# Kernel optimization log

Measured on AMD Instinct MI355X. Metric: run time of the kernel, lower is better.

The kernel has to match this reference:

```python
import jax, jax.numpy as jnp
import numpy as np


def setup_inputs() -> dict:
    key = jax.random.key(0)
    k1, k2, k3, k4, k5 = jax.random.split(key, 5)
    B, S, DK, D = 64, 2048, 1024, 1024
    hidden_state = jax.random.normal(k1, (B, D), dtype=jnp.float32)
    encoder_outputs = jax.random.normal(k2, (B, S, DK), dtype=jnp.float32)
    # linear1: in = dim_key + dim*num_layers = 2048, out = dim = 1024
    W1 = jax.random.normal(k3, (D, DK + D), dtype=jnp.float32) * (1.0 / np.sqrt(DK + D))
    b1 = jax.random.normal(k4, (D,), dtype=jnp.float32) * 0.01
    W2 = jax.random.normal(k5, (1, D), dtype=jnp.float32) * (1.0 / np.sqrt(D))
    return {"hidden_state": hidden_state, "encoder_outputs": encoder_outputs,
            "W1": W1, "b1": b1, "W2": W2}


def reference(hidden_state, encoder_outputs, W1, b1, W2):
    # torch: cat([enc, h], -1) @ W1.T  ==  enc @ W1e.T + h @ W1h.T
    # (split avoids materializing the [B,S,DK+D] concat; same math)
    DK = encoder_outputs.shape[-1]
    W1e, W1h = W1[:, :DK], W1[:, DK:]
    # pre: [B, S, D]
    pre = (jnp.einsum('bsk,dk->bsd', encoder_outputs, W1e)
           + jnp.einsum('bm,dm->bd', hidden_state, W1h)[:, None, :]
           + b1)
    e = jnp.einsum('bsd,d->bs', jnp.tanh(pre), W2[0])  # scores [B, S]
    alpha = jax.nn.softmax(e, axis=1)
    context = jnp.einsum('bs,bsk->bk', alpha, encoder_outputs)  # [B, DK]
    return context
```

## Files before the change

### kernel.cpp

```cpp
#include <hip/hip_runtime.h>

typedef __attribute__((ext_vector_type(8))) short short8;
typedef __attribute__((ext_vector_type(4))) float floatx4;

#define M_TOT 131072
#define SEQ   2048
#define NB    8

__device__ __forceinline__ unsigned bf16rne(float x) {
  unsigned u = __float_as_uint(x);
  return (u + 0x7FFFu + ((u >> 16) & 1u)) >> 16;
}

#define GLOAD_LDS16(g, l) __builtin_amdgcn_global_load_lds( \
    (const __attribute__((address_space(1))) unsigned int*)(g), \
    (__attribute__((address_space(3))) unsigned int*)(l), 16, 0, 0)

__global__ __launch_bounds__(256) void convert_enc_kernel(
    const float* __restrict__ in, unsigned int* __restrict__ out)
{
  size_t i = ((size_t)blockIdx.x * 256 + threadIdx.x) * 8;
  float4 a = *(const float4*)(in + i);
  float4 b = *(const float4*)(in + i + 4);
  uint4 o;
  o.x = bf16rne(a.x) | (bf16rne(a.y) << 16);
  o.y = bf16rne(a.z) | (bf16rne(a.w) << 16);
  o.z = bf16rne(b.x) | (bf16rne(b.y) << 16);
  o.w = bf16rne(b.z) | (bf16rne(b.w) << 16);
  *(uint4*)(out + i / 2) = o;
}

__global__ __launch_bounds__(128) void convert_w1e_kernel(
    const float* __restrict__ W1, unsigned int* __restrict__ out)
{
  int d = blockIdx.x;
  int k = threadIdx.x * 8;
  const float* p = W1 + (size_t)d * 2048 + k;
  float4 a = *(const float4*)p;
  float4 b = *(const float4*)(p + 4);
  uint4 o;
  o.x = bf16rne(a.x) | (bf16rne(a.y) << 16);
  o.y = bf16rne(a.z) | (bf16rne(a.w) << 16);
  o.z = bf16rne(b.x) | (bf16rne(b.y) << 16);
  o.w = bf16rne(b.z) | (bf16rne(b.w) << 16);
  *(uint4*)(out + ((size_t)d * 1024 + k) / 2) = o;
}

__global__ __launch_bounds__(256) void hvec_kernel(
    const float* __restrict__ hid, const float* __restrict__ W1,
    const float* __restrict__ b1, float* __restrict__ hvec)
{
  int b = blockIdx.x, g = blockIdx.y;
  int w = threadIdx.x >> 6, lane = threadIdx.x & 63;
  const float* hrow = hid + b * 1024;
  for (int i = 0; i < 16; ++i) {
    int d = g * 64 + w * 16 + i;
    const float* wrow = W1 + (size_t)d * 2048 + 1024;
    float sum = 0.f;
#pragma unroll
    for (int c = 0; c < 4; ++c) {
      int m = c * 256 + lane * 4;
      float4 wv = *(const float4*)(wrow + m);
      float4 hv = *(const float4*)(hrow + m);
      sum += wv.x * hv.x + wv.y * hv.y + wv.z * hv.z + wv.w * hv.w;
    }
#pragma unroll
    for (int msk = 1; msk < 64; msk <<= 1) sum += __shfl_xor(sum, msk);
    if (lane == 0) hvec[b * 1024 + d] = sum + b1[d];
  }
}

__global__ __launch_bounds__(512, 2) void gemm256_kernel(
    const unsigned short* __restrict__ A, const unsigned short* __restrict__ B,
    const float* __restrict__ W2, const float* __restrict__ hvec,
    float* __restrict__ epart)
{
  __shared__ __align__(16) unsigned short lds[4][2][8192];

  const int tid = threadIdx.x;
  const int lid = blockIdx.x;
  const int xcd = lid & 7, q = lid >> 3;
  const int mb = xcd * 64 + (q >> 2);
  const int nb = q & 3;
  const int r0 = mb * 256, n0 = nb * 256;
  const int bidx = r0 >> 11;
  const int wid = tid >> 6, lane = tid & 63;
  const int wm = wid >> 2, wn = wid & 3;
  const int lrow = lane & 15, kq = lane >> 4;

  int offA[2], offB[2], dst[2];
#pragma unroll
  for (int j = 0; j < 2; ++j) {
    int c = tid + j * 512;
    int r = c >> 2, s = c & 3;
    offA[j] = (r0 + r) * 1024 + s * 8;
    offB[j] = (n0 + r) * 1024 + s * 8;
    dst[j] = (wid * 64 + j * 512) * 8;
  }

  floatx4 acc[8][4];
#pragma unroll
  for (int i = 0; i < 8; ++i)
#pragma unroll
    for (int j = 0; j < 4; ++j)
      acc[i][j] = (floatx4){0.f, 0.f, 0.f, 0.f};

#define STAGE_J(T, J) do { \
    GLOAD_LDS16(A + (size_t)offA[J] + (T) * 32, &lds[(T) & 3][0][dst[J]]); \
    GLOAD_LDS16(B + (size_t)offB[J] + (T) * 32, &lds[(T) & 3][1][dst[J]]); \
  } while (0)

  STAGE_J(0, 0); STAGE_J(0, 1);
  STAGE_J(1, 0); STAGE_J(1, 1);

  const int aB = wm * 4096 + lrow * 32 + kq * 8;
  const int bB = wn * 2048 + lrow * 32 + kq * 8;

  for (int tt = 0; tt < 8; ++tt) {
#pragma unroll
    for (int u = 0; u < 4; ++u) {
      const int t = tt * 4 + u;
      const unsigned short* Ah = lds[u][0];
      const unsigned short* Bh = lds[u][1];

      if (t >= 30) { asm volatile("s_waitcnt vmcnt(0)" ::: "memory"); }
      else         { asm volatile("s_waitcnt vmcnt(4)" ::: "memory"); }
      __builtin_amdgcn_s_barrier();

      short8 af[8];
#pragma unroll
      for (int mt = 0; mt < 8; ++mt) af[mt] = *(const short8*)&Ah[aB + mt * 512];
      short8 bf0 = *(const short8*)&Bh[bB];
      short8 bf1 = *(const short8*)&Bh[bB + 512];
      if (t < 30) STAGE_J(t + 2, 0);
      __builtin_amdgcn_s_setprio(1);
#pragma unroll
      for (int mt = 0; mt < 8; ++mt) {
        acc[mt][0] = __builtin_amdgcn_mfma_f32_16x16x32_bf16(af[mt], bf0, acc[mt][0], 0, 0, 0);
        acc[mt][1] = __builtin_amdgcn_mfma_f32_16x16x32_bf16(af[mt], bf1, acc[mt][1], 0, 0, 0);
      }
      __builtin_amdgcn_s_setprio(0);
      short8 bf2 = *(const short8*)&Bh[bB + 1024];
      short8 bf3 = *(const short8*)&Bh[bB + 1536];
      if (t < 30) STAGE_J(t + 2, 1);
      __builtin_amdgcn_s_setprio(1);
#pragma unroll
      for (int mt = 0; mt < 8; ++mt) {
        acc[mt][2] = __builtin_amdgcn_mfma_f32_16x16x32_bf16(af[mt], bf2, acc[mt][2], 0, 0, 0);
        acc[mt][3] = __builtin_amdgcn_mfma_f32_16x16x32_bf16(af[mt], bf3, acc[mt][3], 0, 0, 0);
      }
      __builtin_amdgcn_s_setprio(0);
    }
  }
#undef STAGE_J

  __syncthreads();
  float* ep = (float*)&lds[0][0][0];
  float hv[4], w2v[4];
#pragma unroll
  for (int nt = 0; nt < 4; ++nt) {
    int n = n0 + wn * 64 + nt * 16 + lrow;
    hv[nt]  = hvec[bidx * 1024 + n];
    w2v[nt] = W2[n];
  }
#pragma unroll
  for (int mt = 0; mt < 8; ++mt) {
#pragma unroll
    for (int r = 0; r < 4; ++r) {
      float sum = 0.f;
#pragma unroll
      for (int nt = 0; nt < 4; ++nt) {
        float pre = acc[mt][nt][r] + hv[nt];
        float ex = __expf(2.f * pre);
        sum += (1.f - 2.f / (ex + 1.f)) * w2v[nt];
      }
      sum += __shfl_xor(sum, 1);
      sum += __shfl_xor(sum, 2);
      sum += __shfl_xor(sum, 4);
      sum += __shfl_xor(sum, 8);
      if (lrow == 0) ep[wn * 256 + wm * 128 + mt * 16 + kq * 4 + r] = sum;
    }
  }
  __syncthreads();
  if (tid < 256) {
    float s = ep[tid] + ep[256 + tid] + ep[512 + tid] + ep[768 + tid];
    epart[(size_t)nb * M_TOT + r0 + tid] = s;
  }
}

__global__ __launch_bounds__(256) void fused_gemm_kernel(
    const float* __restrict__ enc, const float* __restrict__ W1,
    const float* __restrict__ W2, const float* __restrict__ hvec,
    float* __restrict__ epart)
{
  __shared__ __align__(16) unsigned short Ah[128 * 32];
  __shared__ __align__(16) unsigned short Bh[128 * 32];
  __shared__ float ep[2][128];

  const int tid = threadIdx.x;
  const int nb = blockIdx.x, mb = blockIdx.y;
  const int r0 = mb * 128, n0 = nb * 128;
  const int bidx = r0 >> 11;
  const int w = tid >> 6, lane = tid & 63;
  const int wm = w >> 1, wn = w & 1;
  const int lrow = lane & 15, kq = lane >> 4;

  floatx4 acc[4][4];
#pragma unroll
  for (int i = 0; i < 4; ++i)
#pragma unroll
    for (int j = 0; j < 4; ++j)
      acc[i][j] = (floatx4){0.f, 0.f, 0.f, 0.f};

  const int srow = tid >> 3;
  const int scol = (tid & 7) * 4;
  const float* aptr = enc + (size_t)(r0 + srow) * 1024 + scol;
  const float* bptr = W1  + (size_t)(n0 + srow) * 2048 + scol;

  for (int k0 = 0; k0 < 1024; k0 += 32) {
    float4 av[4], bv[4];
#pragma unroll
    for (int j = 0; j < 4; ++j) {
      av[j] = *(const float4*)(aptr + (size_t)(j * 32) * 1024 + k0);
      bv[j] = *(const float4*)(bptr + (size_t)(j * 32) * 2048 + k0);
    }
    __syncthreads();
#pragma unroll
    for (int j = 0; j < 4; ++j) {
      unsigned ax = __float_as_uint(av[j].x), ay = __float_as_uint(av[j].y);
      unsigned az = __float_as_uint(av[j].z), aw = __float_as_uint(av[j].w);
      unsigned a01 = __builtin_amdgcn_perm(ay, ax, 0x07060302u);
      unsigned a23 = __builtin_amdgcn_perm(aw, az, 0x07060302u);
      *(uint2*)&Ah[(tid + j * 256) * 4] = make_uint2(a01, a23);
      unsigned bx = __float_as_uint(bv[j].x), by = __float_as_uint(bv[j].y);
      unsigned bz = __float_as_uint(bv[j].z), bw = __float_as_uint(bv[j].w);
      unsigned b01 = __builtin_amdgcn_perm(by, bx, 0x07060302u);
      unsigned b23 = __builtin_amdgcn_perm(bw, bz, 0x07060302u);
      *(uint2*)&Bh[(tid + j * 256) * 4] = make_uint2(b01, b23);
    }
    __syncthreads();

    short8 af[4], bfm[4];
#pragma unroll
    for (int t4 = 0; t4 < 4; ++t4) {
      af[t4]  = *(const short8*)&Ah[(wm * 64 + t4 * 16 + lrow) * 32 + kq * 8];
      bfm[t4] = *(const short8*)&Bh[(wn * 64 + t4 * 16 + lrow) * 32 + kq * 8];
    }
#pragma unroll
    for (int mt = 0; mt < 4; ++mt)
#pragma unroll
      for (int nt = 0; nt < 4; ++nt)
        acc[mt][nt] = __builtin_amdgcn_mfma_f32_16x16x32_bf16(
            af[mt], bfm[nt], acc[mt][nt], 0, 0, 0);
  }

  float hv[4], w2v[4];
#pragma unroll
  for (int nt = 0; nt < 4; ++nt) {
    int n = n0 + wn * 64 + nt * 16 + lrow;
    hv[nt]  = hvec[bidx * 1024 + n];
    w2v[nt] = W2[n];
  }
#pragma unroll
  for (int mt = 0; mt < 4; ++mt) {
#pragma unroll
    for (int r = 0; r < 4; ++r) {
      float sum = 0.f;
#pragma unroll
      for (int nt = 0; nt < 4; ++nt) {
        float pre = acc[mt][nt][r] + hv[nt];
        float ex = __expf(2.f * pre);
        sum += (1.f - 2.f / (ex + 1.f)) * w2v[nt];
      }
      sum += __shfl_xor(sum, 1);
      sum += __shfl_xor(sum, 2);
      sum += __shfl_xor(sum, 4);
      sum += __shfl_xor(sum, 8);
      if (lrow == 0) ep[wn][wm * 64 + mt * 16 + kq * 4 + r] = sum;
    }
  }
  __syncthreads();
  if (tid < 128)
    epart[(size_t)nb * M_TOT + r0 + tid] = ep[0][tid] + ep[1][tid];
}

template<int NP>
__global__ __launch_bounds__(256) void softmax_kernel(
    const float* __restrict__ epart, float* __restrict__ alpha)
{
  int b = blockIdx.x, t = threadIdx.x;
  __shared__ float redmax[4], redsum[4];
  float ev[8];
  float lmax = -1e30f;
#pragma unroll
  for (int j = 0; j < 8; ++j) {
    int s = t + j * 256;
    float sum = 0.f;
#pragma unroll
    for (int p = 0; p < NP; ++p) sum += epart[(size_t)p * M_TOT + b * SEQ + s];
    ev[j] = sum;
    lmax = fmaxf(lmax, sum);
  }
#pragma unroll
  for (int msk = 1; msk < 64; msk <<= 1) lmax = fmaxf(lmax, __shfl_xor(lmax, msk));
  if ((t & 63) == 0) redmax[t >> 6] = lmax;
  __syncthreads();
  float bmax = fmaxf(fmaxf(redmax[0], redmax[1]), fmaxf(redmax[2], redmax[3]));
  float lsum = 0.f;
#pragma unroll
  for (int j = 0; j < 8; ++j) { ev[j] = __expf(ev[j] - bmax); lsum += ev[j]; }
#pragma unroll
  for (int msk = 1; msk < 64; msk <<= 1) lsum += __shfl_xor(lsum, msk);
  if ((t & 63) == 0) redsum[t >> 6] = lsum;
  __syncthreads();
  float inv = 1.f / (redsum[0] + redsum[1] + redsum[2] + redsum[3]);
#pragma unroll
  for (int j = 0; j < 8; ++j) alpha[b * SEQ + t + j * 256] = ev[j] * inv;
}

__global__ __launch_bounds__(256) void context_bf16_kernel(
    const unsigned int* __restrict__ encB, const float* __restrict__ alpha,
    float* __restrict__ out)
{
  __shared__ float red[8][128];
  int b = blockIdx.x, kc = blockIdx.y, t = threadIdx.x;
  int kl = (t & 31) * 4;
  int strip = t >> 5;
  const unsigned int* ep = encB +
      (((size_t)b * SEQ + strip * 256) * 1024 + kc * 128 + kl) / 2;
  const float* ap = alpha + b * SEQ + strip * 256;
  float a0 = 0.f, a1 = 0.f, a2 = 0.f, a3 = 0.f;
#pragma unroll 4
  for (int s = 0; s < 256; ++s) {
    float a = ap[s];
    uint2 v = *(const uint2*)(ep + (size_t)s * 512);
    a0 += a * __uint_as_float(v.x << 16);
    a1 += a * __uint_as_float(v.x & 0xFFFF0000u);
    a2 += a * __uint_as_float(v.y << 16);
    a3 += a * __uint_as_float(v.y & 0xFFFF0000u);
  }
  red[strip][kl + 0] = a0;
  red[strip][kl + 1] = a1;
  red[strip][kl + 2] = a2;
  red[strip][kl + 3] = a3;
  __syncthreads();
  if (t < 128) {
    float s = 0.f;
#pragma unroll
    for (int j = 0; j < 8; ++j) s += red[j][t];
    out[b * 1024 + kc * 128 + t] = s;
  }
}

__global__ __launch_bounds__(256) void context_kernel(
    const float* __restrict__ enc, const float* __restrict__ alpha,
    float* __restrict__ out)
{
  int b = blockIdx.y, sq = blockIdx.z, t = threadIdx.x;
  int k4 = t * 4;
  const float* ep = enc + ((size_t)b * SEQ + sq * 128) * 1024 + k4;
  const float* ap = alpha + b * SEQ + sq * 128;
  float ax = 0.f, ay = 0.f, az = 0.f, aw = 0.f;
#pragma unroll 4
  for (int s = 0; s < 128; ++s) {
    float a = ap[s];
    float4 v = *(const float4*)(ep + (size_t)s * 1024);
    ax += a * v.x; ay += a * v.y; az += a * v.z; aw += a * v.w;
  }
  float* o = out + b * 1024 + k4;
  atomicAdd(o + 0, ax);
  atomicAdd(o + 1, ay);
  atomicAdd(o + 2, az);
  atomicAdd(o + 3, aw);
}

extern "C" void kernel_launch(void* const* d_in, const int* in_sizes, int n_in,
                              void* d_out, int out_size, void* d_ws, size_t ws_size,
                              hipStream_t stream) {
  const float* hid = (const float*)d_in[0];
  const float* enc = (const float*)d_in[1];
  const float* W1  = (const float*)d_in[2];
  const float* b1  = (const float*)d_in[3];
  const float* W2  = (const float*)d_in[4];
  float* out = (float*)d_out;

  float* epart = (float*)d_ws;
  float* alpha = epart + (size_t)NB * M_TOT;
  float* hvec  = alpha + M_TOT;
  size_t small_bytes = ((size_t)NB * M_TOT + M_TOT + 64 * 1024) * 4;
  size_t encB_off = ((small_bytes + 255) / 256) * 256;
  size_t need = encB_off + (size_t)M_TOT * 1024 * 2 + (size_t)1024 * 1024 * 2;

  hvec_kernel<<<dim3(64, 16), 256, 0, stream>>>(hid, W1, b1, hvec);

  if (ws_size >= need) {
    unsigned short* encB = (unsigned short*)((char*)d_ws + encB_off);
    unsigned short* W1eB = encB + (size_t)M_TOT * 1024;
    convert_enc_kernel<<<65536, 256, 0, stream>>>(enc, (unsigned int*)encB);
    convert_w1e_kernel<<<1024, 128, 0, stream>>>(W1, (unsigned int*)W1eB);
    gemm256_kernel<<<2048, 512, 0, stream>>>(encB, W1eB, W2, hvec, epart);
    softmax_kernel<4><<<64, 256, 0, stream>>>(epart, alpha);
    context_bf16_kernel<<<dim3(64, 8), 256, 0, stream>>>((unsigned int*)encB, alpha, out);
  } else {
    hipMemsetAsync(d_out, 0, (size_t)out_size * sizeof(float), stream);
    fused_gemm_kernel<<<dim3(NB, 1024), 256, 0, stream>>>(enc, W1, W2, hvec, epart);
    softmax_kernel<8><<<64, 256, 0, stream>>>(epart, alpha);
    context_kernel<<<dim3(1, 64, 16), 256, 0, stream>>>(enc, alpha, out);
  }
}
```

Measured before the change: 1.083 ms.

## Restructure GEMM main loop sync and widen hvec/context kernel parallelism

```diff
diff --git a/kernel.cpp b/kernel.cpp
--- a/kernel.cpp
+++ b/kernel.cpp
@@ -53,8 +53,8 @@
   int b = blockIdx.x, g = blockIdx.y;
   int w = threadIdx.x >> 6, lane = threadIdx.x & 63;
   const float* hrow = hid + b * 1024;
-  for (int i = 0; i < 16; ++i) {
-    int d = g * 64 + w * 16 + i;
+  for (int i = 0; i < 4; ++i) {
+    int d = g * 16 + w * 4 + i;
     const float* wrow = W1 + (size_t)d * 2048 + 1024;
     float sum = 0.f;
 #pragma unroll
@@ -116,6 +116,9 @@
   const int aB = wm * 4096 + lrow * 32 + kq * 8;
   const int bB = wn * 2048 + lrow * 32 + kq * 8;
 
+  asm volatile("s_waitcnt vmcnt(4)" ::: "memory");
+  __builtin_amdgcn_s_barrier();
+
   for (int tt = 0; tt < 8; ++tt) {
 #pragma unroll
     for (int u = 0; u < 4; ++u) {
@@ -123,33 +126,41 @@
       const unsigned short* Ah = lds[u][0];
       const unsigned short* Bh = lds[u][1];
 
-      if (t >= 30) { asm volatile("s_waitcnt vmcnt(0)" ::: "memory"); }
-      else         { asm volatile("s_waitcnt vmcnt(4)" ::: "memory"); }
+      short8 af[8], bf[4];
+#pragma unroll
+      for (int mt = 0; mt < 4; ++mt) af[mt] = *(const short8*)&Ah[aB + mt * 512];
+#pragma unroll
+      for (int nt = 0; nt < 4; ++nt) bf[nt] = *(const short8*)&Bh[bB + nt * 512];
+      if (t < 30) STAGE_J(t + 2, 0);
       __builtin_amdgcn_s_barrier();
-
-      short8 af[8];
-#pragma unroll
-      for (int mt = 0; mt < 8; ++mt) af[mt] = *(const short8*)&Ah[aB + mt * 512];
-      short8 bf0 = *(const short8*)&Bh[bB];
-      short8 bf1 = *(const short8*)&Bh[bB + 512];
-      if (t < 30) STAGE_J(t + 2, 0);
+      asm volatile("s_waitcnt lgkmcnt(0)" ::: "memory");
+      __builtin_amdgcn_sched_barrier(0);
       __builtin_amdgcn_s_setprio(1);
 #pragma unroll
-      for (int mt = 0; mt < 8; ++mt) {
-        acc[mt][0] = __builtin_amdgcn_mfma_f32_16x16x32_bf16(af[mt], bf0, acc[mt][0], 0, 0, 0);
-        acc[mt][1] = __builtin_amdgcn_mfma_f32_16x16x32_bf16(af[mt], bf1, acc[mt][1], 0, 0, 0);
-      }
+      for (int mt = 0; mt < 4; ++mt)
+#pragma unroll
+        for (int nt = 0; nt < 4; ++nt)
+          acc[mt][nt] = __builtin_amdgcn_mfma_f32_16x16x32_bf16(
+              af[mt], bf[nt], acc[mt][nt], 0, 0, 0);
       __builtin_amdgcn_s_setprio(0);
-      short8 bf2 = *(const short8*)&Bh[bB + 1024];
-      short8 bf3 = *(const short8*)&Bh[bB + 1536];
+      __builtin_amdgcn_s_barrier();
+#pragma unroll
+      for (int mt = 4; mt < 8; ++mt) af[mt] = *(const short8*)&Ah[aB + mt * 512];
       if (t < 30) STAGE_J(t + 2, 1);
+      __builtin_amdgcn_s_barrier();
+      asm volatile("s_waitcnt lgkmcnt(0)" ::: "memory");
+      __builtin_amdgcn_sched_barrier(0);
       __builtin_amdgcn_s_setprio(1);
 #pragma unroll
-      for (int mt = 0; mt < 8; ++mt) {
-        acc[mt][2] = __builtin_amdgcn_mfma_f32_16x16x32_bf16(af[mt], bf2, acc[mt][2], 0, 0, 0);
-        acc[mt][3] = __builtin_amdgcn_mfma_f32_16x16x32_bf16(af[mt], bf3, acc[mt][3], 0, 0, 0);
-      }
+      for (int mt = 4; mt < 8; ++mt)
+#pragma unroll
+        for (int nt = 0; nt < 4; ++nt)
+          acc[mt][nt] = __builtin_amdgcn_mfma_f32_16x16x32_bf16(
+              af[mt], bf[nt], acc[mt][nt], 0, 0, 0);
       __builtin_amdgcn_s_setprio(0);
+      if (t < 30) { asm volatile("s_waitcnt vmcnt(4)" ::: "memory"); }
+      else        { asm volatile("s_waitcnt vmcnt(0)" ::: "memory"); }
+      __builtin_amdgcn_s_barrier();
     }
   }
 #undef STAGE_J
@@ -318,20 +329,20 @@
   for (int j = 0; j < 8; ++j) alpha[b * SEQ + t + j * 256] = ev[j] * inv;
 }
 
-__global__ __launch_bounds__(256) void context_bf16_kernel(
+__global__ __launch_bounds__(512) void context_bf16_kernel(
     const unsigned int* __restrict__ encB, const float* __restrict__ alpha,
     float* __restrict__ out)
 {
-  __shared__ float red[8][128];
+  __shared__ float red[16][128];
   int b = blockIdx.x, kc = blockIdx.y, t = threadIdx.x;
   int kl = (t & 31) * 4;
   int strip = t >> 5;
   const unsigned int* ep = encB +
-      (((size_t)b * SEQ + strip * 256) * 1024 + kc * 128 + kl) / 2;
-  const float* ap = alpha + b * SEQ + strip * 256;
+      (((size_t)b * SEQ + strip * 128) * 1024 + kc * 128 + kl) / 2;
+  const float* ap = alpha + b * SEQ + strip * 128;
   float a0 = 0.f, a1 = 0.f, a2 = 0.f, a3 = 0.f;
 #pragma unroll 4
-  for (int s = 0; s < 256; ++s) {
+  for (int s = 0; s < 128; ++s) {
     float a = ap[s];
     uint2 v = *(const uint2*)(ep + (size_t)s * 512);
     a0 += a * __uint_as_float(v.x << 16);
@@ -347,7 +358,7 @@
   if (t < 128) {
     float s = 0.f;
 #pragma unroll
-    for (int j = 0; j < 8; ++j) s += red[j][t];
+    for (int j = 0; j < 16; ++j) s += red[j][t];
     out[b * 1024 + kc * 128 + t] = s;
   }
 }
@@ -391,7 +402,7 @@
   size_t encB_off = ((small_bytes + 255) / 256) * 256;
   size_t need = encB_off + (size_t)M_TOT * 1024 * 2 + (size_t)1024 * 1024 * 2;
 
-  hvec_kernel<<<dim3(64, 16), 256, 0, stream>>>(hid, W1, b1, hvec);
+  hvec_kernel<<<dim3(64, 64), 256, 0, stream>>>(hid, W1, b1, hvec);
 
   if (ws_size >= need) {
     unsigned short* encB = (unsigned short*)((char*)d_ws + encB_off);
@@ -400,7 +411,7 @@
     convert_w1e_kernel<<<1024, 128, 0, stream>>>(W1, (unsigned int*)W1eB);
     gemm256_kernel<<<2048, 512, 0, stream>>>(encB, W1eB, W2, hvec, epart);
     softmax_kernel<4><<<64, 256, 0, stream>>>(epart, alpha);
-    context_bf16_kernel<<<dim3(64, 8), 256, 0, stream>>>((unsigned int*)encB, alpha, out);
+    context_bf16_kernel<<<dim3(64, 8), 512, 0, stream>>>((unsigned int*)encB, alpha, out);
   } else {
     hipMemsetAsync(d_out, 0, (size_t)out_size * sizeof(float), stream);
     fused_gemm_kernel<<<dim3(NB, 1024), 256, 0, stream>>>(enc, W1, W2, hvec, epart);
```

Result: no change. 1.091 ms (+0.7%).
